# Performance work log

Measured on AMD Instinct MI355X. Metric: run time of the kernel, lower is better.

The kernel has to match this reference:

```python
import jax, jax.numpy as jnp
import numpy as np

H = 180  # hidden size
T = 240  # timesteps

def lstm_cell_zero_state(x, Wih, bih, bhh):
    # torch nn.LSTMCell called with no (h, c): h = c = 0, so the W_hh term
    # vanishes and f-gate * c_prev vanishes. Gate order in torch: i, f, g, o.
    # x: [B, T, F] -> vectorized over all timesteps at once (no recurrence).
    gates = jnp.einsum('btf,gf->btg', x, Wih) + bih + bhh  # [B, T, 4H]
    i, f, g, o = jnp.split(gates, 4, axis=-1)
    c = jax.nn.sigmoid(i) * jnp.tanh(g)
    h = jax.nn.sigmoid(o) * jnp.tanh(c)
    return h  # [B, T, H]

def setup_inputs() -> dict:
    key = jax.random.key(0)
    ks = jax.random.split(key, 8)
    B = 2048
    s = lambda fan_in: 1.0 / np.sqrt(fan_in)
    x = jax.random.normal(ks[0], (B, 3, 60, T), dtype=jnp.float32)
    # Encoder LSTMCell(180 -> 180)
    W_ih_enc = jax.random.uniform(ks[1], (4 * H, 180), jnp.float32, -s(H), s(H))
    b_ih_enc = jax.random.uniform(ks[2], (4 * H,), jnp.float32, -s(H), s(H))
    b_hh_enc = jax.random.uniform(ks[3], (4 * H,), jnp.float32, -s(H), s(H))
    # Decoder LSTMCell(180 -> 180)
    W_ih_dec = jax.random.uniform(ks[4], (4 * H, H), jnp.float32, -s(H), s(H))
    b_ih_dec = jax.random.uniform(ks[5], (4 * H,), jnp.float32, -s(H), s(H))
    b_hh_dec = jax.random.uniform(ks[6], (4 * H,), jnp.float32, -s(H), s(H))
    # Output Linear(240*180 -> 40)
    W_out = jax.random.uniform(ks[7], (40, T * H), jnp.float32, -s(T * H), s(T * H))
    b_out = jnp.zeros((40,), jnp.float32)
    return {"x": x, "W_ih_enc": W_ih_enc, "b_ih_enc": b_ih_enc, "b_hh_enc": b_hh_enc,
            "W_ih_dec": W_ih_dec, "b_ih_dec": b_ih_dec, "b_hh_dec": b_hh_dec,
            "W_out": W_out, "b_out": b_out}

def reference(x, W_ih_enc, b_ih_enc, b_hh_enc, W_ih_dec, b_ih_dec, b_hh_dec, W_out, b_out):
    B = x.shape[0]
    # Encoder: [B,3,60,240] -> [B,240,3,60] -> [B,240,180]
    xe = jnp.transpose(x, (0, 3, 1, 2)).reshape(B, T, 3 * 60)
    h_enc = lstm_cell_zero_state(xe, W_ih_enc, b_ih_enc, b_hh_enc)  # [B,T,H]
    enc = jax.nn.softmax(h_enc, axis=2)
    # Decoder LSTM (also zero-state every step)
    h_dec = lstm_cell_zero_state(enc, W_ih_dec, b_ih_dec, b_hh_dec)  # [B,T,H]
    flat = h_dec.reshape(B, T * H)
    logits = flat @ W_out.T + b_out  # [B,40]
    out = jax.nn.softmax(logits.reshape(B, 4, 10), axis=2)
    return out
```

## Files before the change

### kernel.cpp

```cpp
#include <hip/hip_runtime.h>
#include <hip/hip_bf16.h>

#define HH 180
#define TT 240
#define KP 192
#define MP 576
#define KOUT 43200
#define BB 2048

#define NCOL 128
#define KD 96
#define NW 12
#define ATHR 768

typedef __attribute__((ext_vector_type(8))) short short8;
typedef __attribute__((ext_vector_type(4))) float float4v;

__device__ inline unsigned short f2bf(float f) {
    unsigned u = __builtin_bit_cast(unsigned, f);
    u += 0x7fffu + ((u >> 16) & 1u);
    return (unsigned short)(u >> 16);
}
__device__ inline unsigned pack_bf2(float a, float b) {
    union { __hip_bfloat162 h; unsigned u; } t;
    t.h = __float22bfloat162_rn(make_float2(a, b));
    return t.u;
}
__device__ inline float sigm(float x) {
    return __builtin_amdgcn_rcpf(1.f + __expf(-x));
}
__device__ inline float tanh_(float x) {
    return 2.f * __builtin_amdgcn_rcpf(1.f + __expf(-2.f * x)) - 1.f;
}

__global__ void prep_kernel(const float* __restrict__ W1, const float* __restrict__ bi1,
                            const float* __restrict__ bh1, const float* __restrict__ W2,
                            const float* __restrict__ bi2, const float* __restrict__ bh2,
                            const float* __restrict__ Wo,
                            unsigned short* __restrict__ W1p, unsigned short* __restrict__ W2p,
                            float* __restrict__ bEp, float* __restrict__ bDp,
                            unsigned short* __restrict__ Wop, float* __restrict__ logits)
{
    int id = blockIdx.x * 256 + threadIdx.x;
    if (id < MP * KP) {
        int mp = id / KP, k = id % KP;
        int g = mp / KP, h = mp % KP;
        unsigned short v1 = 0, v2 = 0;
        if (h < HH && k < HH) {
            int r = (g == 0) ? h : (g == 1 ? 360 + h : 540 + h);
            v1 = f2bf(W1[r * HH + k]);
            v2 = f2bf(W2[r * HH + k]);
        }
        W1p[id] = v1; W2p[id] = v2;
    }
    if (id < MP) {
        int g = id / KP, h = id % KP;
        float v1 = 0.f, v2 = 0.f;
        if (h < HH) {
            int r = (g == 0) ? h : (g == 1 ? 360 + h : 540 + h);
            v1 = bi1[r] + bh1[r];
            v2 = bi2[r] + bh2[r];
        }
        bEp[id] = v1; bDp[id] = v2;
    }
    if (id < 48 * KOUT) {
        int n = id / KOUT, k = id % KOUT;
        Wop[id] = (n < 40) ? f2bf(Wo[n * KOUT + k]) : (unsigned short)0;
    }
    if (id < BB * 40) logits[id] = 0.f;
}

__global__ __launch_bounds__(ATHR, 3) void phaseA_kernel(
    const float* __restrict__ x, const unsigned short* __restrict__ W1p,
    const unsigned short* __restrict__ W2p, const float* __restrict__ bEp,
    const float* __restrict__ bDp, unsigned short* __restrict__ hdec)
{
    __shared__ __align__(16) unsigned XsD[NCOL * KD];
    __shared__ __align__(16) unsigned EsD[NCOL * KD];
    __shared__ float bEs[MP], bDs[MP];
    __shared__ float sred2[NCOL];

    const int tid = threadIdx.x;
    const int b = blockIdx.x >> 1;
    const int t0 = (blockIdx.x & 1) * 112;
    const float* xb = x + (size_t)b * HH * TT;

    for (int i = tid; i < MP; i += ATHR) { bEs[i] = bEp[i]; bDs[i] = bDp[i]; }
    if (tid < NCOL) sred2[tid] = 0.f;

    {
        const int c = tid & (NCOL - 1), q = tid >> 7;
        const int swz = (c & 7) << 2;
        const int cbase = c * KD;
        #pragma unroll
        for (int j = 0; j < 15; ++j) {
            int p = q + 6 * j;
            float a0 = xb[(size_t)(2 * p) * TT + t0 + c];
            float a1 = xb[(size_t)(2 * p + 1) * TT + t0 + c];
            XsD[(cbase + p) ^ swz] = pack_bf2(a0, a1);
        }
        XsD[(cbase + 90 + q) ^ swz] = 0u;
    }

    const int lane = tid & 63, wv = tid >> 6;
    const int l15 = lane & 15, l4 = lane >> 4;
    const int h0 = wv * 16 + l4 * 4;

    const uint4* W1q = (const uint4*)W1p;
    const uint4* W2q = (const uint4*)W2p;
    short8 Af[3][6];
    #pragma unroll
    for (int sec = 0; sec < 3; ++sec) {
        int rowbase = (sec * KP + wv * 16 + l15) * (KP / 8) + l4;
        #pragma unroll
        for (int ks = 0; ks < 6; ++ks) {
            union { uint4 q; short8 v; } a;
            a.q = W1q[rowbase + ks * 4];
            Af[sec][ks] = a.v;
        }
    }
    __syncthreads();

    float bi_[4], bg_[4], bo_[4];
    #pragma unroll
    for (int e = 0; e < 4; ++e) {
        bi_[e] = bEs[h0 + e];
        bg_[e] = bEs[KP + h0 + e];
        bo_[e] = bEs[2 * KP + h0 + e];
    }

    for (int ct = 0; ct < 8; ++ct) {
        const int col = ct * 16 + l15;
        const int swz = (col & 7) << 2;
        const int bb = col * KD + l4 * 4;
        short8 Bf[6];
        #pragma unroll
        for (int ks = 0; ks < 6; ++ks) {
            union { uint4 q; short8 v; } t;
            t.q = *(const uint4*)&XsD[(bb + ks * 16) ^ swz];
            Bf[ks] = t.v;
        }
        float4v acc[3];
        acc[0] = (float4v){0.f, 0.f, 0.f, 0.f};
        acc[1] = (float4v){0.f, 0.f, 0.f, 0.f};
        acc[2] = (float4v){0.f, 0.f, 0.f, 0.f};
        #pragma unroll
        for (int ks = 0; ks < 6; ++ks) {
            acc[0] = __builtin_amdgcn_mfma_f32_16x16x32_bf16(Af[0][ks], Bf[ks], acc[0], 0, 0, 0);
            acc[1] = __builtin_amdgcn_mfma_f32_16x16x32_bf16(Af[1][ks], Bf[ks], acc[1], 0, 0, 0);
            acc[2] = __builtin_amdgcn_mfma_f32_16x16x32_bf16(Af[2][ks], Bf[ks], acc[2], 0, 0, 0);
        }
        float ev[4], es = 0.f;
        #pragma unroll
        for (int e = 0; e < 4; ++e) {
            float gi = acc[0][e] + bi_[e];
            float gg = acc[1][e] + bg_[e];
            float go = acc[2][e] + bo_[e];
            float cc = sigm(gi) * tanh_(gg);
            ev[e] = __expf(sigm(go) * tanh_(cc));
            es += (h0 + e < HH) ? ev[e] : 0.f;
        }
        {
            int kd = (col * KD + (h0 >> 1)) ^ swz;
            uint2 pv;
            pv.x = pack_bf2(ev[0], ev[1]);
            pv.y = pack_bf2(ev[2], ev[3]);
            *(uint2*)&EsD[kd] = pv;
        }
        es += __shfl_xor(es, 16);
        es += __shfl_xor(es, 32);
        if (lane < 16) atomicAdd(&sred2[ct * 16 + lane], es);
    }

    #pragma unroll
    for (int sec = 0; sec < 3; ++sec) {
        int rowbase = (sec * KP + wv * 16 + l15) * (KP / 8) + l4;
        #pragma unroll
        for (int ks = 0; ks < 6; ++ks) {
            union { uint4 q; short8 v; } a;
            a.q = W2q[rowbase + ks * 4];
            Af[sec][ks] = a.v;
        }
    }
    __syncthreads();

    #pragma unroll
    for (int e = 0; e < 4; ++e) {
        bi_[e] = bDs[h0 + e];
        bg_[e] = bDs[KP + h0 + e];
        bo_[e] = bDs[2 * KP + h0 + e];
    }

    unsigned short* hout = hdec + (size_t)b * TT * HH;
    for (int ct = 0; ct < 8; ++ct) {
        const int col = ct * 16 + l15;
        const int swz = (col & 7) << 2;
        const int bb = col * KD + l4 * 4;
        short8 Bf[6];
        #pragma unroll
        for (int ks = 0; ks < 6; ++ks) {
            union { uint4 q; short8 v; } t;
            t.q = *(const uint4*)&EsD[(bb + ks * 16) ^ swz];
            Bf[ks] = t.v;
        }
        float4v acc[3];
        acc[0] = (float4v){0.f, 0.f, 0.f, 0.f};
        acc[1] = (float4v){0.f, 0.f, 0.f, 0.f};
        acc[2] = (float4v){0.f, 0.f, 0.f, 0.f};
        #pragma unroll
        for (int ks = 0; ks < 6; ++ks) {
            acc[0] = __builtin_amdgcn_mfma_f32_16x16x32_bf16(Af[0][ks], Bf[ks], acc[0], 0, 0, 0);
            acc[1] = __builtin_amdgcn_mfma_f32_16x16x32_bf16(Af[1][ks], Bf[ks], acc[1], 0, 0, 0);
            acc[2] = __builtin_amdgcn_mfma_f32_16x16x32_bf16(Af[2][ks], Bf[ks], acc[2], 0, 0, 0);
        }
        if (h0 < HH) {
            float rsv = __builtin_amdgcn_rcpf(sred2[col]);
            float o[4];
            #pragma unroll
            for (int e = 0; e < 4; ++e) {
                float gi = acc[0][e] * rsv + bi_[e];
                float gg = acc[1][e] * rsv + bg_[e];
                float go = acc[2][e] * rsv + bo_[e];
                float cc = sigm(gi) * tanh_(gg);
                o[e] = sigm(go) * tanh_(cc);
            }
            uint2 pv;
            pv.x = pack_bf2(o[0], o[1]);
            pv.y = pack_bf2(o[2], o[3]);
            *(uint2*)(hout + (size_t)(t0 + col) * HH + h0) = pv;
        }
    }
}

__global__ __launch_bounds__(256, 4) void phaseB_kernel(
    const unsigned short* __restrict__ hdec, const unsigned short* __restrict__ Wop,
    float* __restrict__ logits)
{
    const int tid = threadIdx.x;
    const int lane = tid & 63, wv = tid >> 6;
    const int l15 = lane & 15, l4 = lane >> 4;
    const int m0 = blockIdx.x * 64 + wv * 16;
    const int k0 = blockIdx.y * 1440;

    const uint4* Aq = (const uint4*)hdec;
    const uint4* Bq = (const uint4*)Wop;
    const int QK = KOUT / 8;
    int abase = (m0 + l15) * QK + (k0 >> 3) + l4;
    int bbase = l15 * QK + (k0 >> 3) + l4;

    float4v acc[3];
    #pragma unroll
    for (int n = 0; n < 3; ++n) acc[n] = (float4v){0.f, 0.f, 0.f, 0.f};

    #pragma unroll 3
    for (int ks = 0; ks < 45; ++ks) {
        union { uint4 q; short8 v; } a, b0, b1, b2;
        a.q  = Aq[abase + ks * 4];
        b0.q = Bq[bbase + ks * 4];
        b1.q = Bq[bbase + 16 * QK + ks * 4];
        b2.q = Bq[bbase + 32 * QK + ks * 4];
        acc[0] = __builtin_amdgcn_mfma_f32_16x16x32_bf16(a.v, b0.v, acc[0], 0, 0, 0);
        acc[1] = __builtin_amdgcn_mfma_f32_16x16x32_bf16(a.v, b1.v, acc[1], 0, 0, 0);
        acc[2] = __builtin_amdgcn_mfma_f32_16x16x32_bf16(a.v, b2.v, acc[2], 0, 0, 0);
    }

    #pragma unroll
    for (int nt = 0; nt < 3; ++nt) {
        int o = nt * 16 + l15;
        if (o < 40) {
            #pragma unroll
            for (int e = 0; e < 4; ++e) {
                int row = m0 + l4 * 4 + e;
                atomicAdd(&logits[row * 40 + o], acc[nt][e]);
            }
        }
    }
}

__global__ void out_kernel(const float* __restrict__ logits, const float* __restrict__ bout,
                           float* __restrict__ out)
{
    int id = blockIdx.x * 256 + threadIdx.x;
    if (id >= BB * 4) return;
    int b = id >> 2, j = id & 3;
    float v[10], mx = -1e30f;
    #pragma unroll
    for (int d = 0; d < 10; ++d) {
        v[d] = logits[b * 40 + j * 10 + d] + bout[j * 10 + d];
        mx = fmaxf(mx, v[d]);
    }
    float s = 0.f;
    #pragma unroll
    for (int d = 0; d < 10; ++d) { v[d] = __expf(v[d] - mx); s += v[d]; }
    float r = __builtin_amdgcn_rcpf(s);
    #pragma unroll
    for (int d = 0; d < 10; ++d) out[b * 40 + j * 10 + d] = v[d] * r;
}

extern "C" void kernel_launch(void* const* d_in, const int* in_sizes, int n_in,
                              void* d_out, int out_size, void* d_ws, size_t ws_size,
                              hipStream_t stream)
{
    const float* x    = (const float*)d_in[0];
    const float* W1   = (const float*)d_in[1];
    const float* bi1  = (const float*)d_in[2];
    const float* bh1  = (const float*)d_in[3];
    const float* W2   = (const float*)d_in[4];
    const float* bi2  = (const float*)d_in[5];
    const float* bh2  = (const float*)d_in[6];
    const float* Wo   = (const float*)d_in[7];
    const float* bout = (const float*)d_in[8];

    char* ws = (char*)d_ws;
    unsigned short* W1p = (unsigned short*)(ws + 0);
    unsigned short* W2p = (unsigned short*)(ws + 221184);
    float* bEp          = (float*)(ws + 442368);
    float* bDp          = (float*)(ws + 444928);
    unsigned short* Wop = (unsigned short*)(ws + 447488);
    float* logits       = (float*)(ws + 4594688);
    unsigned short* hdec= (unsigned short*)(ws + 4922368);

    prep_kernel<<<(48 * KOUT + 255) / 256, 256, 0, stream>>>(
        W1, bi1, bh1, W2, bi2, bh2, Wo, W1p, W2p, bEp, bDp, Wop, logits);
    phaseA_kernel<<<BB * 2, ATHR, 0, stream>>>(x, W1p, W2p, bEp, bDp, hdec);
    phaseB_kernel<<<dim3(32, 30), 256, 0, stream>>>(hdec, Wop, logits);
    out_kernel<<<(BB * 4 + 255) / 256, 256, 0, stream>>>(logits, bout, (float*)d_out);
}
```

Before: 955.4 us.

## Retile phase A to 80 columns and fuse LSTM activations with Padé tanh

```diff
diff --git a/kernel.cpp b/kernel.cpp
--- a/kernel.cpp
+++ b/kernel.cpp
@@ -8,7 +8,7 @@
 #define KOUT 43200
 #define BB 2048
 
-#define NCOL 128
+#define NCOL 80
 #define KD 96
 #define NW 12
 #define ATHR 768
@@ -26,11 +26,13 @@
     t.h = __float22bfloat162_rn(make_float2(a, b));
     return t.u;
 }
-__device__ inline float sigm(float x) {
-    return __builtin_amdgcn_rcpf(1.f + __expf(-x));
-}
-__device__ inline float tanh_(float x) {
-    return 2.f * __builtin_amdgcn_rcpf(1.f + __expf(-2.f * x)) - 1.f;
+
+__device__ inline float lstm_act(float pa, float pb, float po) {
+    float cc  = (1.f - pb) * __builtin_amdgcn_rcpf((1.f + pa) * (1.f + pb));
+    float x2  = cc * cc;
+    float num = cc * (x2 * (x2 + 105.f) + 945.f);
+    float den = x2 * (x2 * 15.f + 420.f) + 945.f;
+    return num * __builtin_amdgcn_rcpf(den * (1.f + po));
 }
 
 __global__ void prep_kernel(const float* __restrict__ W1, const float* __restrict__ bi1,
@@ -81,25 +83,25 @@
     __shared__ float sred2[NCOL];
 
     const int tid = threadIdx.x;
-    const int b = blockIdx.x >> 1;
-    const int t0 = (blockIdx.x & 1) * 112;
+    const int b = blockIdx.y;
+    const int t0 = blockIdx.x * NCOL;
     const float* xb = x + (size_t)b * HH * TT;
 
     for (int i = tid; i < MP; i += ATHR) { bEs[i] = bEp[i]; bDs[i] = bDp[i]; }
     if (tid < NCOL) sred2[tid] = 0.f;
 
-    {
-        const int c = tid & (NCOL - 1), q = tid >> 7;
-        const int swz = (c & 7) << 2;
-        const int cbase = c * KD;
-        #pragma unroll
-        for (int j = 0; j < 15; ++j) {
-            int p = q + 6 * j;
+    #pragma unroll
+    for (int it = 0; it < 10; ++it) {
+        int i = it * ATHR + tid;
+        int p = i / NCOL;
+        int c = i - p * NCOL;
+        unsigned v = 0u;
+        if (p < 90) {
             float a0 = xb[(size_t)(2 * p) * TT + t0 + c];
             float a1 = xb[(size_t)(2 * p + 1) * TT + t0 + c];
-            XsD[(cbase + p) ^ swz] = pack_bf2(a0, a1);
-        }
-        XsD[(cbase + 90 + q) ^ swz] = 0u;
+            v = pack_bf2(a0, a1);
+        }
+        XsD[(c * KD + p) ^ ((c & 7) << 2)] = v;
     }
 
     const int lane = tid & 63, wv = tid >> 6;
@@ -121,15 +123,16 @@
     }
     __syncthreads();
 
-    float bi_[4], bg_[4], bo_[4];
+    float nbi[4], nbg[4], nbo[4];
     #pragma unroll
     for (int e = 0; e < 4; ++e) {
-        bi_[e] = bEs[h0 + e];
-        bg_[e] = bEs[KP + h0 + e];
-        bo_[e] = bEs[2 * KP + h0 + e];
-    }
-
-    for (int ct = 0; ct < 8; ++ct) {
+        nbi[e] = -bEs[h0 + e];
+        nbg[e] = -2.f * bEs[KP + h0 + e];
+        nbo[e] = -bEs[2 * KP + h0 + e];
+    }
+
+    #pragma unroll 1
+    for (int ct = 0; ct < 5; ++ct) {
         const int col = ct * 16 + l15;
         const int swz = (col & 7) << 2;
         const int bb = col * KD + l4 * 4;
@@ -153,11 +156,11 @@
         float ev[4], es = 0.f;
         #pragma unroll
         for (int e = 0; e < 4; ++e) {
-            float gi = acc[0][e] + bi_[e];
-            float gg = acc[1][e] + bg_[e];
-            float go = acc[2][e] + bo_[e];
-            float cc = sigm(gi) * tanh_(gg);
-            ev[e] = __expf(sigm(go) * tanh_(cc));
+            float pa = __expf(fmaf(acc[0][e], -1.f, nbi[e]));
+            float pb = __expf(fmaf(acc[1][e], -2.f, nbg[e]));
+            float po = __expf(fmaf(acc[2][e], -1.f, nbo[e]));
+            float hv = lstm_act(pa, pb, po);
+            ev[e] = __expf(hv);
             es += (h0 + e < HH) ? ev[e] : 0.f;
         }
         {
@@ -186,13 +189,14 @@
 
     #pragma unroll
     for (int e = 0; e < 4; ++e) {
-        bi_[e] = bDs[h0 + e];
-        bg_[e] = bDs[KP + h0 + e];
-        bo_[e] = bDs[2 * KP + h0 + e];
+        nbi[e] = -bDs[h0 + e];
+        nbg[e] = -2.f * bDs[KP + h0 + e];
+        nbo[e] = -bDs[2 * KP + h0 + e];
     }
 
     unsigned short* hout = hdec + (size_t)b * TT * HH;
-    for (int ct = 0; ct < 8; ++ct) {
+    #pragma unroll 1
+    for (int ct = 0; ct < 5; ++ct) {
         const int col = ct * 16 + l15;
         const int swz = (col & 7) << 2;
         const int bb = col * KD + l4 * 4;
@@ -214,15 +218,15 @@
             acc[2] = __builtin_amdgcn_mfma_f32_16x16x32_bf16(Af[2][ks], Bf[ks], acc[2], 0, 0, 0);
         }
         if (h0 < HH) {
-            float rsv = __builtin_amdgcn_rcpf(sred2[col]);
+            float nrs  = -__builtin_amdgcn_rcpf(sred2[col]);
+            float nrs2 = nrs + nrs;
             float o[4];
             #pragma unroll
             for (int e = 0; e < 4; ++e) {
-                float gi = acc[0][e] * rsv + bi_[e];
-                float gg = acc[1][e] * rsv + bg_[e];
-                float go = acc[2][e] * rsv + bo_[e];
-                float cc = sigm(gi) * tanh_(gg);
-                o[e] = sigm(go) * tanh_(cc);
+                float pa = __expf(fmaf(acc[0][e], nrs,  nbi[e]));
+                float pb = __expf(fmaf(acc[1][e], nrs2, nbg[e]));
+                float po = __expf(fmaf(acc[2][e], nrs,  nbo[e]));
+                o[e] = lstm_act(pa, pb, po);
             }
             uint2 pv;
             pv.x = pack_bf2(o[0], o[1]);
@@ -252,7 +256,7 @@
     #pragma unroll
     for (int n = 0; n < 3; ++n) acc[n] = (float4v){0.f, 0.f, 0.f, 0.f};
 
-    #pragma unroll 3
+    #pragma unroll 5
     for (int ks = 0; ks < 45; ++ks) {
         union { uint4 q; short8 v; } a, b0, b1, b2;
         a.q  = Aq[abase + ks * 4];
@@ -322,7 +326,7 @@
 
     prep_kernel<<<(48 * KOUT + 255) / 256, 256, 0, stream>>>(
         W1, bi1, bh1, W2, bi2, bh2, Wo, W1p, W2p, bEp, bDp, Wop, logits);
-    phaseA_kernel<<<BB * 2, ATHR, 0, stream>>>(x, W1p, W2p, bEp, bDp, hdec);
+    phaseA_kernel<<<dim3(3, BB), ATHR, 0, stream>>>(x, W1p, W2p, bEp, bDp, hdec);
     phaseB_kernel<<<dim3(32, 30), 256, 0, stream>>>(hdec, Wop, logits);
     out_kernel<<<(BB * 4 + 255) / 256, 256, 0, stream>>>(logits, bout, (float*)d_out);
 }
```

Result: no change. 970.3 us (+1.6%).
